# Kernel tuning notes

Hardware: AMD Instinct MI355X
Metric: run time of the kernel (lower is better)

The kernel has to match this reference:

```python
import jax, jax.numpy as jnp
import numpy as np
from jax import lax

B, N, M, K = 8, 4096, 2048, 64   # graphs, points/graph, fps centers/graph (ratio=0.5), max neighbors
R = 0.5                           # radius
F_IN = 64


def setup_inputs() -> dict:
    key = jax.random.key(0)
    ks = jax.random.split(key, 6)
    x = jax.random.normal(ks[0], (B * N, F_IN), jnp.float32)
    pos = jax.random.normal(ks[1], (B * N, 3), jnp.float32)
    batch = jnp.repeat(jnp.arange(B, dtype=jnp.int32), N)  # sorted graph ids
    def lin_w(k, fi, fo):
        return (jax.random.normal(k, (fi, fo), jnp.float32) / np.sqrt(fi)).astype(jnp.float32)
    w1 = lin_w(ks[2], F_IN + 3, 64); b1 = jnp.zeros((64,), jnp.float32)
    w2 = lin_w(ks[3], 64, 64);       b2 = jnp.zeros((64,), jnp.float32)
    w3 = lin_w(ks[4], 64, 128);      b3 = jnp.zeros((128,), jnp.float32)
    return dict(x=x, pos=pos, batch=batch, w1=w1, b1=b1, w2=w2, b2=b2, w3=w3, b3=b3)


def fps(pos_g, m):
    """Farthest point sampling on one graph [n,3] -> m int32 indices (deterministic start at 0)."""
    n = pos_g.shape[0]
    def step(carry, _):
        mind, last = carry
        d = jnp.sum((pos_g - pos_g[last]) ** 2, axis=-1)
        mind = jnp.minimum(mind, d)
        return (mind, jnp.argmax(mind).astype(jnp.int32)), last
    init = (jnp.full((n,), 1e30, jnp.float32), jnp.int32(0))
    _, idx = lax.scan(step, init, None, length=m)
    return idx


def reference(x, pos, batch, w1, b1, w2, b2, w3, b3):
    # batch is sorted with equal-size graphs -> reshape to [B, N, .]
    pos_b = pos.reshape(B, N, 3)
    x_b = x.reshape(B, N, F_IN)

    # fps per graph (PyG.fps with ratio=0.5)
    cidx = jax.vmap(lambda p: fps(p, M))(pos_b)                 # [B, M]
    bi = jnp.arange(B)[:, None]
    pos_c = pos_b[bi, cidx]                                     # [B, M, 3]

    # radius ball query, capped at K neighbors (take K nearest, mask > R)
    d2 = jnp.sum((pos_c[:, :, None, :] - pos_b[:, None, :, :]) ** 2, axis=-1)  # [B, M, N]
    neg_d2k, nbr = lax.top_k(-d2, K)                            # [B, M, K]
    mask = (-neg_d2k) <= R * R                                  # center itself always valid (d=0)

    # PointConv message: nn(concat[x_j, pos_j - pos_i]), then max-aggregate per center
    bii = jnp.arange(B)[:, None, None]
    x_j = x_b[bii, nbr]                                         # [B, M, K, F_IN]
    rel = pos_b[bii, nbr] - pos_c[:, :, None, :]                # [B, M, K, 3]
    h = jnp.concatenate([x_j, rel], axis=-1)                    # [B, M, K, F_IN+3]
    h = jax.nn.relu(h @ w1 + b1)
    h = jax.nn.relu(h @ w2 + b2)
    h = h @ w3 + b3                                             # [B, M, K, 128]
    h = jnp.where(mask[..., None], h, -jnp.inf)
    out = jnp.max(h, axis=2)                                    # [B, M, 128]

    out_x = out.reshape(B * M, 128)
    out_pos = pos_c.reshape(B * M, 3)
    out_batch = jnp.repeat(jnp.arange(B, dtype=jnp.int32), M)
    return out_x, out_pos, out_batch
```

## Files before the change

kernel.cpp:

```cpp
#include <hip/hip_runtime.h>

#define BG 8
#define NP 4096
#define MC 2048
#define KN 64
#define NWK 248
#define CAND 480

__device__ __forceinline__ float dist2(float ax, float ay, float az,
                                       float bx, float by, float bz) {
    float dx = __fsub_rn(ax, bx), dy = __fsub_rn(ay, by), dz = __fsub_rn(az, bz);
    return __fadd_rn(__fadd_rn(__fmul_rn(dx, dx), __fmul_rn(dy, dy)), __fmul_rn(dz, dz));
}

template <int CTRL>
__device__ __forceinline__ float dppmax(float v) {
    int t = __builtin_amdgcn_update_dpp(0, __float_as_int(v), CTRL, 0xf, 0xf, true);
    return fmaxf(v, __int_as_float(t));
}

__global__ __launch_bounds__(512, 1) void k_fused(
    const float* __restrict__ pos, const float* __restrict__ x,
    const float* __restrict__ w1, const float* __restrict__ b1,
    const float* __restrict__ w2, const float* __restrict__ b2,
    const float* __restrict__ w3, const float* __restrict__ b3,
    float* __restrict__ y,
    float* __restrict__ out_pos, float* __restrict__ out_batch, float* __restrict__ out_x,
    int* __restrict__ prog, int* __restrict__ yready)
{
    __shared__ float smem[24576];
    const int tid = threadIdx.x;
    if (blockIdx.x < BG) {
        const int b = blockIdx.x;
        const float* pg = pos + (size_t)b * NP * 3;
        for (int i = tid; i < NP * 3; i += 512) smem[i] = pg[i];
        __syncthreads();
        const int lane = tid & 63, wv = tid >> 6;
        float px[8], py[8], pz[8], mind[8];
        const int base = tid * 8;
        #pragma unroll
        for (int i = 0; i < 8; i++) {
            px[i] = smem[(base + i) * 3];
            py[i] = smem[(base + i) * 3 + 1];
            pz[i] = smem[(base + i) * 3 + 2];
            mind[i] = 1e30f;
        }
        float2* sl = (float2*)(smem + NP * 3);
        float cx = smem[0], cy = smem[1], cz = smem[2];
        if (tid == 0) {
            const size_t c3 = (size_t)b * MC * 3;
            __hip_atomic_store(&out_pos[c3 + 0], cx, __ATOMIC_RELAXED, __HIP_MEMORY_SCOPE_AGENT);
            __hip_atomic_store(&out_pos[c3 + 1], cy, __ATOMIC_RELAXED, __HIP_MEMORY_SCOPE_AGENT);
            __hip_atomic_store(&out_pos[c3 + 2], cz, __ATOMIC_RELAXED, __HIP_MEMORY_SCOPE_AGENT);
        }
        for (int m = 1; m < MC; m++) {
            float bv = -1.0f; int bi = base;
            #pragma unroll
            for (int i = 0; i < 8; i++) {
                float d = dist2(px[i], py[i], pz[i], cx, cy, cz);
                float nm = fminf(mind[i], d);
                mind[i] = nm;
                if (nm > bv) { bv = nm; bi = base + i; }
            }
            float v = bv;
            v = dppmax<0x111>(v);
            v = dppmax<0x112>(v);
            v = dppmax<0x114>(v);
            v = dppmax<0x118>(v);
            v = dppmax<0x142>(v);
            v = dppmax<0x143>(v);
            const float V = __int_as_float(__builtin_amdgcn_readlane(__float_as_int(v), 63));
            unsigned long long mk = __ballot(bv == V);
            float2* sb = sl + (m & 1) * 8;
            if (lane == (int)(__ffsll((long long)mk) - 1))
                sb[wv] = make_float2(V, __int_as_float(bi));
            __syncthreads();
            const float4* sq = (const float4*)sb;
            float4 q0 = sq[0], q1 = sq[1], q2 = sq[2], q3 = sq[3];
            float Vg = q0.x; int ig = __float_as_int(q0.y);
            if (q0.z > Vg) { Vg = q0.z; ig = __float_as_int(q0.w); }
            if (q1.x > Vg) { Vg = q1.x; ig = __float_as_int(q1.y); }
            if (q1.z > Vg) { Vg = q1.z; ig = __float_as_int(q1.w); }
            if (q2.x > Vg) { Vg = q2.x; ig = __float_as_int(q2.y); }
            if (q2.z > Vg) { Vg = q2.z; ig = __float_as_int(q2.w); }
            if (q3.x > Vg) { Vg = q3.x; ig = __float_as_int(q3.y); }
            if (q3.z > Vg) { Vg = q3.z; ig = __float_as_int(q3.w); }
            cx = smem[ig * 3]; cy = smem[ig * 3 + 1]; cz = smem[ig * 3 + 2];
            if (tid == 0) {
                const size_t c3 = (size_t)(b * MC + m) * 3;
                __hip_atomic_store(&out_pos[c3 + 0], cx, __ATOMIC_RELAXED, __HIP_MEMORY_SCOPE_AGENT);
                __hip_atomic_store(&out_pos[c3 + 1], cy, __ATOMIC_RELAXED, __HIP_MEMORY_SCOPE_AGENT);
                __hip_atomic_store(&out_pos[c3 + 2], cz, __ATOMIC_RELAXED, __HIP_MEMORY_SCOPE_AGENT);
                __hip_atomic_store(&prog[b * 16], m, __ATOMIC_RELAXED, __HIP_MEMORY_SCOPE_AGENT);
            }
        }
        __syncthreads();
        if (tid == 0)
            __hip_atomic_store(&prog[b * 16], MC, __ATOMIC_RELEASE, __HIP_MEMORY_SCOPE_AGENT);
        for (int i = tid; i < MC; i += 512) out_batch[b * MC + i] = (float)b;
    } else {
        const int w = blockIdx.x - BG;
        const int g = w & 7;
        const int sub = w >> 3;
        const int lane = tid & 63, ww = tid >> 6;
        const int waveid = sub * 8 + ww;
        float* wsm = smem;
        for (int i = tid; i < 4096; i += 512) wsm[i] = w1[i];
        const float b1v = b1[lane];
        __syncthreads();
        const int p0 = sub * 133;
        const int p1 = (p0 + 133 < NP) ? p0 + 133 : NP;
        const float* xg = x + (size_t)g * NP * 64;
        float* yg_w = y + (size_t)g * NP * 64;
        for (int p = p0 + ww; p < p1; p += 8) {
            float xrow = xg[(size_t)p * 64 + lane];
            float acc = b1v;
            #pragma unroll
            for (int f = 0; f < 64; f++) {
                float xf = __shfl(xrow, f, 64);
                acc = fmaf(xf, wsm[f * 64 + lane], acc);
            }
            yg_w[(size_t)p * 64 + lane] = acc;
        }
        __syncthreads();
        if (tid == 0)
            __hip_atomic_fetch_add(&yready[g * 16], 1, __ATOMIC_RELEASE, __HIP_MEMORY_SCOPE_AGENT);
        float w2c[64], w3a[64], w3b[64];
        #pragma unroll
        for (int f = 0; f < 64; f++) {
            w2c[f] = w2[f * 64 + lane];
            w3a[f] = w3[f * 128 + lane];
            w3b[f] = w3[f * 128 + 64 + lane];
        }
        const float b2v = b2[lane], b3av = b3[lane], b3bv = b3[lane + 64];
        const float wp0 = w1[64 * 64 + lane], wp1 = w1[65 * 64 + lane], wp2 = w1[66 * 64 + lane];
        while (__hip_atomic_load(&yready[g * 16], __ATOMIC_RELAXED, __HIP_MEMORY_SCOPE_AGENT) < 31)
            __builtin_amdgcn_s_sleep(16);
        {
            int yr = __hip_atomic_load(&yready[g * 16], __ATOMIC_ACQUIRE, __HIP_MEMORY_SCOPE_AGENT);
            asm volatile("" :: "v"(yr));
        }
        float2* cand = (float2*)(smem + 4096) + ww * CAND;
        int* nlist = (int*)(smem + 11776) + ww * 64;
        float* st1 = smem + 12288 + ww * 136;
        float* st2 = st1 + 68;
        const float* pg = pos + (size_t)g * NP * 3;
        const float* yg = y + (size_t)g * NP * 64;
        for (int m = waveid; m < MC; m += NWK) {
            int cur;
            while ((cur = __hip_atomic_load(&prog[g * 16], __ATOMIC_RELAXED, __HIP_MEMORY_SCOPE_AGENT)) <= m) {
                if (m - cur > 16) __builtin_amdgcn_s_sleep(64);
                else              __builtin_amdgcn_s_sleep(4);
            }
            const int ci = g * MC + m;
            const size_t c3 = (size_t)ci * 3;
            const float cx = __hip_atomic_load(&out_pos[c3 + 0], __ATOMIC_RELAXED, __HIP_MEMORY_SCOPE_AGENT);
            const float cy = __hip_atomic_load(&out_pos[c3 + 1], __ATOMIC_RELAXED, __HIP_MEMORY_SCOPE_AGENT);
            const float cz = __hip_atomic_load(&out_pos[c3 + 2], __ATOMIC_RELAXED, __HIP_MEMORY_SCOPE_AGENT);
            int cnt = 0;
            for (int c = 0; c < 64; c++) {
                const int p = c * 64 + lane;
                float ppx = pg[p * 3], ppy = pg[p * 3 + 1], ppz = pg[p * 3 + 2];
                float d2 = dist2(ppx, ppy, ppz, cx, cy, cz);
                bool inr = d2 <= 0.25f;
                unsigned long long mk = __ballot(inr);
                int pre = __popcll(mk & ((1ull << lane) - 1ull));
                int wp = cnt + pre;
                if (inr && wp < CAND) cand[wp] = make_float2(d2, __int_as_float(p));
                cnt += __popcll(mk);
            }
            if (cnt > CAND) cnt = CAND;
            int kc;
            if (cnt <= KN) {
                kc = cnt;
                if (lane < cnt) nlist[lane] = __float_as_int(cand[lane].y);
            } else {
                kc = KN;
                for (int basej = 0; basej < cnt; basej += 64) {
                    int jj = basej + lane;
                    float dj = 3.4e38f; int ij = 0x7fffffff;
                    bool act = jj < cnt;
                    if (act) { float2 e = cand[jj]; dj = e.x; ij = __float_as_int(e.y); }
                    int rank = 0;
                    for (int l = 0; l < cnt; l++) {
                        float2 e = cand[l];
                        float dl = e.x; int il = __float_as_int(e.y);
                        if (dl < dj || (dl == dj && il < ij)) rank++;
                    }
                    if (act && rank < KN) nlist[rank] = ij;
                }
            }
            float mA = -3.4e38f, mB = -3.4e38f;
            for (int k = 0; k < kc; k++) {
                const int j = nlist[k];
                const float yv = yg[(size_t)j * 64 + lane];
                const float jx = pg[j * 3], jy = pg[j * 3 + 1], jz = pg[j * 3 + 2];
                float rx = jx - cx, ry = jy - cy, rz = jz - cz;
                float h1 = fmaf(rx, wp0, yv);
                h1 = fmaf(ry, wp1, h1);
                h1 = fmaf(rz, wp2, h1);
                h1 = fmaxf(h1, 0.f);
                st1[lane] = h1;
                float a2a = b2v, a2b = 0.f;
                #pragma unroll
                for (int fc = 0; fc < 16; fc += 2) {
                    float4 hA = *(const float4*)&st1[fc * 4];
                    float4 hB = *(const float4*)&st1[fc * 4 + 4];
                    a2a = fmaf(hA.x, w2c[fc * 4], a2a);
                    a2a = fmaf(hA.y, w2c[fc * 4 + 1], a2a);
                    a2a = fmaf(hA.z, w2c[fc * 4 + 2], a2a);
                    a2a = fmaf(hA.w, w2c[fc * 4 + 3], a2a);
                    a2b = fmaf(hB.x, w2c[fc * 4 + 4], a2b);
                    a2b = fmaf(hB.y, w2c[fc * 4 + 5], a2b);
                    a2b = fmaf(hB.z, w2c[fc * 4 + 6], a2b);
                    a2b = fmaf(hB.w, w2c[fc * 4 + 7], a2b);
                }
                float h2 = fmaxf(a2a + a2b, 0.f);
                st2[lane] = h2;
                float a3 = b3av, a4 = b3bv;
                #pragma unroll
                for (int fc = 0; fc < 16; fc++) {
                    float4 h = *(const float4*)&st2[fc * 4];
                    a3 = fmaf(h.x, w3a[fc * 4], a3);
                    a3 = fmaf(h.y, w3a[fc * 4 + 1], a3);
                    a3 = fmaf(h.z, w3a[fc * 4 + 2], a3);
                    a3 = fmaf(h.w, w3a[fc * 4 + 3], a3);
                    a4 = fmaf(h.x, w3b[fc * 4], a4);
                    a4 = fmaf(h.y, w3b[fc * 4 + 1], a4);
                    a4 = fmaf(h.z, w3b[fc * 4 + 2], a4);
                    a4 = fmaf(h.w, w3b[fc * 4 + 3], a4);
                }
                mA = fmaxf(mA, a3);
                mB = fmaxf(mB, a4);
            }
            out_x[(size_t)ci * 128 + lane] = mA;
            out_x[(size_t)ci * 128 + 64 + lane] = mB;
        }
    }
}

extern "C" void kernel_launch(void* const* d_in, const int* in_sizes, int n_in,
                              void* d_out, int out_size, void* d_ws, size_t ws_size,
                              hipStream_t stream) {
    const float* x   = (const float*)d_in[0];
    const float* pos = (const float*)d_in[1];
    const float* w1  = (const float*)d_in[3];
    const float* b1  = (const float*)d_in[4];
    const float* w2  = (const float*)d_in[5];
    const float* b2  = (const float*)d_in[6];
    const float* w3  = (const float*)d_in[7];
    const float* b3  = (const float*)d_in[8];

    float* out_x     = (float*)d_out;
    float* out_pos   = out_x + (size_t)BG * MC * 128;
    float* out_batch = out_pos + (size_t)BG * MC * 3;

    char* ws    = (char*)d_ws;
    float* y    = (float*)ws;
    int* prog   = (int*)(ws + 8388608);
    int* yready = (int*)(ws + 8389120);

    (void)hipMemsetAsync(prog, 0, 1024, stream);
    hipLaunchKernelGGL(k_fused, dim3(256), dim3(512), 0, stream,
                       pos, x, w1, b1, w2, b2, w3, b3,
                       y, out_pos, out_batch, out_x, prog, yready);
}
```

Before: 1.364 ms.

## Spatially sort FPS points into cells and skip waves whose bounds cannot change

Reorders each graph's points by a Morton-like cell code so that every thread holds spatially coherent points. A bounding-sphere test per iteration lets whole waves skip the distance update when the new center cannot lower any of their minimum distances. The winning position is now carried through the reductions with a lexicographic index tie-break, which removes the dependent shared-memory load of the center. This adds setup cost (histogram, scan, scatter), more DPP traffic per reduction, and relies on the bound test staying conservative under rounding.

Result: slower. 3.230 ms (+136.9%).

```diff
diff --git a/kernel.cpp b/kernel.cpp
--- a/kernel.cpp
+++ b/kernel.cpp
@@ -13,10 +13,18 @@
     return __fadd_rn(__fadd_rn(__fmul_rn(dx, dx), __fmul_rn(dy, dy)), __fmul_rn(dz, dz));
 }
 
+#define LEXSTEP(CTRL) { \
+    float ov = __int_as_float(__builtin_amdgcn_update_dpp(__float_as_int(v),  __float_as_int(v),  CTRL, 0xf, 0xf, false)); \
+    int   oi = __builtin_amdgcn_update_dpp(ii, ii, CTRL, 0xf, 0xf, false); \
+    float ox = __int_as_float(__builtin_amdgcn_update_dpp(__float_as_int(fx), __float_as_int(fx), CTRL, 0xf, 0xf, false)); \
+    float oy = __int_as_float(__builtin_amdgcn_update_dpp(__float_as_int(fy), __float_as_int(fy), CTRL, 0xf, 0xf, false)); \
+    float oz = __int_as_float(__builtin_amdgcn_update_dpp(__float_as_int(fz), __float_as_int(fz), CTRL, 0xf, 0xf, false)); \
+    bool tk = (ov > v) || (ov == v && oi < ii); \
+    v = tk ? ov : v; ii = tk ? oi : ii; fx = tk ? ox : fx; fy = tk ? oy : fy; fz = tk ? oz : fz; }
+
 template <int CTRL>
-__device__ __forceinline__ float dppmax(float v) {
-    int t = __builtin_amdgcn_update_dpp(0, __float_as_int(v), CTRL, 0xf, 0xf, true);
-    return fmaxf(v, __int_as_float(t));
+__device__ __forceinline__ float dppmov0(float x) {
+    return __int_as_float(__builtin_amdgcn_update_dpp(0, __float_as_int(x), CTRL, 0xf, 0xf, true));
 }
 
 __global__ __launch_bounds__(512, 1) void k_fused(
@@ -33,20 +41,69 @@
     if (blockIdx.x < BG) {
         const int b = blockIdx.x;
         const float* pg = pos + (size_t)b * NP * 3;
-        for (int i = tid; i < NP * 3; i += 512) smem[i] = pg[i];
-        __syncthreads();
-        const int lane = tid & 63, wv = tid >> 6;
+        float* posL = smem;
+        int* srcidx = (int*)(smem + 12288);
+        int* hist   = (int*)(smem + 16384);
+        int* cursor = (int*)(smem + 16896);
+        float4* slotA = (float4*)(smem + 17472);
+        float*  slotB = smem + 17536;
+        for (int i = tid; i < NP * 3; i += 512) posL[i] = pg[i];
+        hist[tid] = 0;
+        __syncthreads();
+        const int lane = tid & 63, wq = tid >> 6;
+        int cells[8];
+        {
+            const float SC = 8.0f / 12.0f;
+            #pragma unroll
+            for (int i = 0; i < 8; i++) {
+                const int p = tid * 8 + i;
+                float xx = posL[p * 3], yy = posL[p * 3 + 1], zz = posL[p * 3 + 2];
+                int cxi = (int)((xx + 6.0f) * SC); cxi = cxi < 0 ? 0 : (cxi > 7 ? 7 : cxi);
+                int cyi = (int)((yy + 6.0f) * SC); cyi = cyi < 0 ? 0 : (cyi > 7 ? 7 : cyi);
+                int czi = (int)((zz + 6.0f) * SC); czi = czi < 0 ? 0 : (czi > 7 ? 7 : czi);
+                cells[i] = (((cxi >> 2) & 1) << 8) | (((cyi >> 2) & 1) << 7) | (((czi >> 2) & 1) << 6)
+                         | (((cxi >> 1) & 1) << 5) | (((cyi >> 1) & 1) << 4) | (((czi >> 1) & 1) << 3)
+                         | ((cxi & 1) << 2) | ((cyi & 1) << 1) | (czi & 1);
+            }
+        }
+        #pragma unroll
+        for (int i = 0; i < 8; i++) atomicAdd(&hist[cells[i]], 1);
+        __syncthreads();
+        int orig = hist[tid];
+        for (int off = 1; off < 512; off <<= 1) {
+            int t = (tid >= off) ? hist[tid - off] : 0;
+            __syncthreads();
+            hist[tid] += t;
+            __syncthreads();
+        }
+        cursor[tid] = hist[tid] - orig;
+        __syncthreads();
+        #pragma unroll
+        for (int i = 0; i < 8; i++) {
+            int dst = atomicAdd(&cursor[cells[i]], 1);
+            srcidx[dst] = tid * 8 + i;
+        }
+        __syncthreads();
         float px[8], py[8], pz[8], mind[8];
-        const int base = tid * 8;
+        int pidx[8];
         #pragma unroll
         for (int i = 0; i < 8; i++) {
-            px[i] = smem[(base + i) * 3];
-            py[i] = smem[(base + i) * 3 + 1];
-            pz[i] = smem[(base + i) * 3 + 2];
+            const int s = srcidx[tid * 8 + i];
+            pidx[i] = s;
+            px[i] = posL[s * 3]; py[i] = posL[s * 3 + 1]; pz[i] = posL[s * 3 + 2];
             mind[i] = 1e30f;
         }
-        float2* sl = (float2*)(smem + NP * 3);
-        float cx = smem[0], cy = smem[1], cz = smem[2];
+        float gx = 0.f, gy = 0.f, gz = 0.f;
+        #pragma unroll
+        for (int i = 0; i < 8; i++) { gx += px[i]; gy += py[i]; gz += pz[i]; }
+        gx *= 0.125f; gy *= 0.125f; gz *= 0.125f;
+        float gr2 = 0.f;
+        #pragma unroll
+        for (int i = 0; i < 8; i++) gr2 = fmaxf(gr2, dist2(px[i], py[i], pz[i], gx, gy, gz));
+        const float gr = sqrtf(gr2) * 1.001f + 1e-6f;
+        float lv = 1e30f;
+        float wV = -1.f, wx = 0.f, wy = 0.f, wz = 0.f; int wI = 0;
+        float cx = posL[0], cy = posL[1], cz = posL[2];
         if (tid == 0) {
             const size_t c3 = (size_t)b * MC * 3;
             __hip_atomic_store(&out_pos[c3 + 0], cx, __ATOMIC_RELAXED, __HIP_MEMORY_SCOPE_AGENT);
@@ -54,38 +111,67 @@
             __hip_atomic_store(&out_pos[c3 + 2], cz, __ATOMIC_RELAXED, __HIP_MEMORY_SCOPE_AGENT);
         }
         for (int m = 1; m < MC; m++) {
-            float bv = -1.0f; int bi = base;
-            #pragma unroll
-            for (int i = 0; i < 8; i++) {
-                float d = dist2(px[i], py[i], pz[i], cx, cy, cz);
-                float nm = fminf(mind[i], d);
-                mind[i] = nm;
-                if (nm > bv) { bv = nm; bi = base + i; }
-            }
-            float v = bv;
-            v = dppmax<0x111>(v);
-            v = dppmax<0x112>(v);
-            v = dppmax<0x114>(v);
-            v = dppmax<0x118>(v);
-            v = dppmax<0x142>(v);
-            v = dppmax<0x143>(v);
-            const float V = __int_as_float(__builtin_amdgcn_readlane(__float_as_int(v), 63));
-            unsigned long long mk = __ballot(bv == V);
-            float2* sb = sl + (m & 1) * 8;
-            if (lane == (int)(__ffsll((long long)mk) - 1))
-                sb[wv] = make_float2(V, __int_as_float(bi));
+            float d2c = dist2(gx, gy, gz, cx, cy, cz);
+            float sd  = sqrtf(d2c) * 0.999f;
+            float rhs = (gr + sqrtf(lv)) * 1.001f + 1e-6f;
+            unsigned long long am = __ballot(!(sd > rhs));
+            const int db = (m & 1) * 8;
+            if (am) {
+                float bv = -1.f; int bi = 0; float bx = cx, by = cy, bz = cz;
+                #pragma unroll
+                for (int i = 0; i < 8; i++) {
+                    float d = dist2(px[i], py[i], pz[i], cx, cy, cz);
+                    float nm = fminf(mind[i], d);
+                    mind[i] = nm;
+                    bool t = (nm > bv) || (nm == bv && pidx[i] < bi);
+                    bv = t ? nm : bv; bi = t ? pidx[i] : bi;
+                    bx = t ? px[i] : bx; by = t ? py[i] : by; bz = t ? pz[i] : bz;
+                }
+                lv = bv;
+                float v = bv, fx = bx, fy = by, fz = bz; int ii = bi;
+                LEXSTEP(0x111)
+                LEXSTEP(0x112)
+                LEXSTEP(0x114)
+                LEXSTEP(0x118)
+                LEXSTEP(0x142)
+                LEXSTEP(0x143)
+                if (lane == 63) { wV = v; wI = ii; wx = fx; wy = fy; wz = fz; }
+            }
+            if (lane == 63) {
+                slotA[db + wq] = make_float4(wV, __int_as_float(wI), wx, wy);
+                slotB[db + wq] = wz;
+            }
             __syncthreads();
-            const float4* sq = (const float4*)sb;
-            float4 q0 = sq[0], q1 = sq[1], q2 = sq[2], q3 = sq[3];
-            float Vg = q0.x; int ig = __float_as_int(q0.y);
-            if (q0.z > Vg) { Vg = q0.z; ig = __float_as_int(q0.w); }
-            if (q1.x > Vg) { Vg = q1.x; ig = __float_as_int(q1.y); }
-            if (q1.z > Vg) { Vg = q1.z; ig = __float_as_int(q1.w); }
-            if (q2.x > Vg) { Vg = q2.x; ig = __float_as_int(q2.y); }
-            if (q2.z > Vg) { Vg = q2.z; ig = __float_as_int(q2.w); }
-            if (q3.x > Vg) { Vg = q3.x; ig = __float_as_int(q3.y); }
-            if (q3.z > Vg) { Vg = q3.z; ig = __float_as_int(q3.w); }
-            cx = smem[ig * 3]; cy = smem[ig * 3 + 1]; cz = smem[ig * 3 + 2];
+            float4 s = slotA[db + (lane & 7)];
+            float sz = slotB[db + (lane & 7)];
+            {
+                float oV = dppmov0<0xB1>(s.x), oI = dppmov0<0xB1>(s.y);
+                float ox = dppmov0<0xB1>(s.z), oy = dppmov0<0xB1>(s.w), oz = dppmov0<0xB1>(sz);
+                bool tk = (oV > s.x) || (oV == s.x && __float_as_int(oI) < __float_as_int(s.y));
+                s.x = tk ? oV : s.x; s.y = tk ? oI : s.y;
+                s.z = tk ? ox : s.z; s.w = tk ? oy : s.w; sz = tk ? oz : sz;
+            }
+            {
+                float oV = dppmov0<0x4E>(s.x), oI = dppmov0<0x4E>(s.y);
+                float ox = dppmov0<0x4E>(s.z), oy = dppmov0<0x4E>(s.w), oz = dppmov0<0x4E>(sz);
+                bool tk = (oV > s.x) || (oV == s.x && __float_as_int(oI) < __float_as_int(s.y));
+                s.x = tk ? oV : s.x; s.y = tk ? oI : s.y;
+                s.z = tk ? ox : s.z; s.w = tk ? oy : s.w; sz = tk ? oz : sz;
+            }
+            {
+                const bool hi = (lane & 4) != 0;
+                float oVl = dppmov0<0x104>(s.x), oVr = dppmov0<0x114>(s.x);
+                float oIl = dppmov0<0x104>(s.y), oIr = dppmov0<0x114>(s.y);
+                float oxl = dppmov0<0x104>(s.z), oxr = dppmov0<0x114>(s.z);
+                float oyl = dppmov0<0x104>(s.w), oyr = dppmov0<0x114>(s.w);
+                float ozl = dppmov0<0x104>(sz),  ozr = dppmov0<0x114>(sz);
+                float oV = hi ? oVr : oVl, oI = hi ? oIr : oIl;
+                float ox = hi ? oxr : oxl, oy = hi ? oyr : oyl, oz = hi ? ozr : ozl;
+                bool tk = (oV > s.x) || (oV == s.x && __float_as_int(oI) < __float_as_int(s.y));
+                s.x = tk ? oV : s.x; s.y = tk ? oI : s.y;
+                s.z = tk ? ox : s.z; s.w = tk ? oy : s.w; sz = tk ? oz : sz;
+            }
+            cx = s.z; cy = s.w; cz = sz;
             if (tid == 0) {
                 const size_t c3 = (size_t)(b * MC + m) * 3;
                 __hip_atomic_store(&out_pos[c3 + 0], cx, __ATOMIC_RELAXED, __HIP_MEMORY_SCOPE_AGENT);
```

## Carry winner coordinates in FPS reduction slots and batch center position stores

Applied to the files above, without the earlier changes.

Each wave's winning lane now writes its value together with the winner's coordinates into a float4 slot. After the barrier, the cross-wave argmax is done with DPP lane exchanges instead of every thread scanning all eight slots and then doing a dependent LDS lookup of the chosen point. Thread 0 also buffers center positions in registers and writes them to global memory in groups of four, and updates the progress counter less often. This shortens the serial critical path of each of the 2048 FPS iterations. In exchange, consumers see progress updates with a lag of up to a few centers, and tie-breaking now depends on lane-order logic in the DPP reduction.

Measured after the change: 1.467 ms. 7.6% more time.

```diff
diff --git a/kernel.cpp b/kernel.cpp
--- a/kernel.cpp
+++ b/kernel.cpp
@@ -17,6 +17,10 @@
 __device__ __forceinline__ float dppmax(float v) {
     int t = __builtin_amdgcn_update_dpp(0, __float_as_int(v), CTRL, 0xf, 0xf, true);
     return fmaxf(v, __int_as_float(t));
+}
+template <int CTRL>
+__device__ __forceinline__ float dppmov(float v) {
+    return __int_as_float(__builtin_amdgcn_update_dpp(0, __float_as_int(v), CTRL, 0xf, 0xf, true));
 }
 
 __global__ __launch_bounds__(512, 1) void k_fused(
@@ -45,8 +49,11 @@
             pz[i] = smem[(base + i) * 3 + 2];
             mind[i] = 1e30f;
         }
-        float2* sl = (float2*)(smem + NP * 3);
+        float4* slotA = (float4*)(smem + NP * 3);
         float cx = smem[0], cy = smem[1], cz = smem[2];
+        float b0x = cx, b0y = cy, b0z = cz;
+        float b1x = 0.f, b1y = 0.f, b1z = 0.f;
+        float b2x = 0.f, b2y = 0.f, b2z = 0.f;
         if (tid == 0) {
             const size_t c3 = (size_t)b * MC * 3;
             __hip_atomic_store(&out_pos[c3 + 0], cx, __ATOMIC_RELAXED, __HIP_MEMORY_SCOPE_AGENT);
@@ -71,27 +78,65 @@
             v = dppmax<0x143>(v);
             const float V = __int_as_float(__builtin_amdgcn_readlane(__float_as_int(v), 63));
             unsigned long long mk = __ballot(bv == V);
-            float2* sb = sl + (m & 1) * 8;
-            if (lane == (int)(__ffsll((long long)mk) - 1))
-                sb[wv] = make_float2(V, __int_as_float(bi));
+            const int db = (m & 1) * 8;
+            if (lane == (int)(__ffsll((long long)mk) - 1)) {
+                float wx = smem[bi * 3], wy = smem[bi * 3 + 1], wz = smem[bi * 3 + 2];
+                slotA[db + wv] = make_float4(bv, wx, wy, wz);
+            }
             __syncthreads();
-            const float4* sq = (const float4*)sb;
-            float4 q0 = sq[0], q1 = sq[1], q2 = sq[2], q3 = sq[3];
-            float Vg = q0.x; int ig = __float_as_int(q0.y);
-            if (q0.z > Vg) { Vg = q0.z; ig = __float_as_int(q0.w); }
-            if (q1.x > Vg) { Vg = q1.x; ig = __float_as_int(q1.y); }
-            if (q1.z > Vg) { Vg = q1.z; ig = __float_as_int(q1.w); }
-            if (q2.x > Vg) { Vg = q2.x; ig = __float_as_int(q2.y); }
-            if (q2.z > Vg) { Vg = q2.z; ig = __float_as_int(q2.w); }
-            if (q3.x > Vg) { Vg = q3.x; ig = __float_as_int(q3.y); }
-            if (q3.z > Vg) { Vg = q3.z; ig = __float_as_int(q3.w); }
-            cx = smem[ig * 3]; cy = smem[ig * 3 + 1]; cz = smem[ig * 3 + 2];
+            float4 s = slotA[db + (lane & 7)];
+            {
+                float oV = dppmov<0xB1>(s.x), ox = dppmov<0xB1>(s.y);
+                float oy = dppmov<0xB1>(s.z), oz = dppmov<0xB1>(s.w);
+                bool tk = (oV > s.x) || ((lane & 1) && oV == s.x);
+                s.x = tk ? oV : s.x; s.y = tk ? ox : s.y;
+                s.z = tk ? oy : s.z; s.w = tk ? oz : s.w;
+            }
+            {
+                float oV = dppmov<0x4E>(s.x), ox = dppmov<0x4E>(s.y);
+                float oy = dppmov<0x4E>(s.z), oz = dppmov<0x4E>(s.w);
+                bool tk = (oV > s.x) || ((lane & 2) && oV == s.x);
+                s.x = tk ? oV : s.x; s.y = tk ? ox : s.y;
+                s.z = tk ? oy : s.z; s.w = tk ? oz : s.w;
+            }
+            {
+                const bool hi = (lane & 4) != 0;
+                float oVl = dppmov<0x104>(s.x), oVr = dppmov<0x114>(s.x);
+                float oxl = dppmov<0x104>(s.y), oxr = dppmov<0x114>(s.y);
+                float oyl = dppmov<0x104>(s.z), oyr = dppmov<0x114>(s.z);
+                float ozl = dppmov<0x104>(s.w), ozr = dppmov<0x114>(s.w);
+                float oV = hi ? oVr : oVl, ox = hi ? oxr : oxl;
+                float oy = hi ? oyr : oyl, oz = hi ? ozr : ozl;
+                bool tk = (oV > s.x) || (hi && oV == s.x);
+                s.x = tk ? oV : s.x; s.y = tk ? ox : s.y;
+                s.z = tk ? oy : s.z; s.w = tk ? oz : s.w;
+            }
+            cx = s.y; cy = s.z; cz = s.w;
             if (tid == 0) {
-                const size_t c3 = (size_t)(b * MC + m) * 3;
-                __hip_atomic_store(&out_pos[c3 + 0], cx, __ATOMIC_RELAXED, __HIP_MEMORY_SCOPE_AGENT);
-                __hip_atomic_store(&out_pos[c3 + 1], cy, __ATOMIC_RELAXED, __HIP_MEMORY_SCOPE_AGENT);
-                __hip_atomic_store(&out_pos[c3 + 2], cz, __ATOMIC_RELAXED, __HIP_MEMORY_SCOPE_AGENT);
-                __hip_atomic_store(&prog[b * 16], m, __ATOMIC_RELAXED, __HIP_MEMORY_SCOPE_AGENT);
+                const int sel = m & 3;
+                if (sel == 0) {
+                    b0x = cx; b0y = cy; b0z = cz;
+                    if (m >= 4)
+                        __hip_atomic_store(&prog[b * 16], m, __ATOMIC_RELAXED, __HIP_MEMORY_SCOPE_AGENT);
+                } else if (sel == 1) {
+                    b1x = cx; b1y = cy; b1z = cz;
+                } else if (sel == 2) {
+                    b2x = cx; b2y = cy; b2z = cz;
+                } else {
+                    const size_t c3 = (size_t)(b * MC + m - 3) * 3;
+                    __hip_atomic_store(&out_pos[c3 + 0],  b0x, __ATOMIC_RELAXED, __HIP_MEMORY_SCOPE_AGENT);
+                    __hip_atomic_store(&out_pos[c3 + 1],  b0y, __ATOMIC_RELAXED, __HIP_MEMORY_SCOPE_AGENT);
+                    __hip_atomic_store(&out_pos[c3 + 2],  b0z, __ATOMIC_RELAXED, __HIP_MEMORY_SCOPE_AGENT);
+                    __hip_atomic_store(&out_pos[c3 + 3],  b1x, __ATOMIC_RELAXED, __HIP_MEMORY_SCOPE_AGENT);
+                    __hip_atomic_store(&out_pos[c3 + 4],  b1y, __ATOMIC_RELAXED, __HIP_MEMORY_SCOPE_AGENT);
+                    __hip_atomic_store(&out_pos[c3 + 5],  b1z, __ATOMIC_RELAXED, __HIP_MEMORY_SCOPE_AGENT);
+                    __hip_atomic_store(&out_pos[c3 + 6],  b2x, __ATOMIC_RELAXED, __HIP_MEMORY_SCOPE_AGENT);
+                    __hip_atomic_store(&out_pos[c3 + 7],  b2y, __ATOMIC_RELAXED, __HIP_MEMORY_SCOPE_AGENT);
+                    __hip_atomic_store(&out_pos[c3 + 8],  b2z, __ATOMIC_RELAXED, __HIP_MEMORY_SCOPE_AGENT);
+                    __hip_atomic_store(&out_pos[c3 + 9],  cx,  __ATOMIC_RELAXED, __HIP_MEMORY_SCOPE_AGENT);
+                    __hip_atomic_store(&out_pos[c3 + 10], cy,  __ATOMIC_RELAXED, __HIP_MEMORY_SCOPE_AGENT);
+                    __hip_atomic_store(&out_pos[c3 + 11], cz,  __ATOMIC_RELAXED, __HIP_MEMORY_SCOPE_AGENT);
+                }
             }
         }
         __syncthreads();
```
